# Optimization experiments

Measured on AMD Instinct MI355X. Metric: run time of the kernel, lower is better.

The kernel has to match this reference:

```python
import jax, jax.numpy as jnp
import numpy as np

# Object condensation loss config (matches init_kwargs / HGCalML defaults)
Q_MIN = 0.5
S_B = 1.0
POT_SCALE = 1.0
REP_SCALE = 1.0
BETA_SCALE = 1.0
E_WEIGHT = 1.0
HUBER_DELTA = 2.0
E_DEN_OFFSET = 1.0
K_MAX = 192          # object-id slots per event; id 0 = noise
EPS = 1e-6

B, N = 4, 50000


def setup_inputs() -> dict:
    key = jax.random.key(0)
    k1, k2, k3, k4, k5 = jax.random.split(key, 5)
    return {
        "beta": jax.random.uniform(k1, (B, N, 1), dtype=jnp.float32),
        "ccoords": jax.random.normal(k2, (B, N, 2), dtype=jnp.float32),
        "pred_energy": jax.random.uniform(k3, (B, N, 1), dtype=jnp.float32),
        "true_energy": jax.random.uniform(k4, (B, N, 1), dtype=jnp.float32),
        "truth_idx": jax.random.randint(k5, (B, N), 0, K_MAX, dtype=jnp.int32),
    }


def _per_event(beta, ccoords, pred_e, true_e, tidx):
    # beta: [N,1], ccoords: [N,2], tidx: [N] int (0 = noise)
    beta = jnp.clip(beta[:, 0], 1e-4, 1.0 - 1e-4)            # [N]
    q = jnp.arctanh(beta) ** 2 + Q_MIN                        # charge  [N]

    ids = jnp.arange(K_MAX)
    M = (tidx[:, None] == ids[None, :]) & (ids[None, :] > 0)  # [N,K] membership
    Mf = M.astype(q.dtype)
    obj_valid = jnp.any(M, axis=0)                            # [K]
    vf = obj_valid.astype(q.dtype)

    # condensation point alpha_k = argmax_q over members of object k
    qM = jnp.where(M, q[:, None], -1.0)                       # [N,K]
    idx_alpha = jnp.argmax(qM, axis=0)                        # [K]
    x_alpha = ccoords[idx_alpha]                              # [K,2]
    q_alpha = q[idx_alpha]                                    # [K]
    beta_alpha = beta[idx_alpha]                              # [K]

    # pairwise hit<->condensation-point distances
    d2 = jnp.sum((ccoords[:, None, :] - x_alpha[None, :, :]) ** 2, axis=-1)  # [N,K]

    # attractive potential (members), repulsive hinge (non-members of valid objects)
    att = jnp.sum(d2 * q_alpha[None, :] * Mf, axis=-1)                       # [N]
    dist = jnp.sqrt(d2 + EPS)
    rep = jnp.sum(jnp.maximum(0.0, 1.0 - dist) * q_alpha[None, :]
                  * (1.0 - Mf) * vf[None, :], axis=-1)                       # [N]
    L_V = jnp.mean(q * (POT_SCALE * att + REP_SCALE * rep))

    n_obj = jnp.sum(vf) + EPS
    L_beta = BETA_SCALE * jnp.sum((1.0 - beta_alpha) * vf) / n_obj

    noise = (tidx == 0).astype(q.dtype)
    L_noise = S_B * jnp.sum(beta * noise) / (jnp.sum(noise) + EPS)

    # energy payload loss: relative error, Huber, beta-weighted per object
    ediff = (pred_e[:, 0] - true_e[:, 0]) / (true_e[:, 0] + E_DEN_OFFSET)
    ad = jnp.abs(ediff)
    eh = jnp.where(ad <= HUBER_DELTA, 0.5 * ad ** 2,
                   HUBER_DELTA * (ad - 0.5 * HUBER_DELTA))                   # [N]
    pw = Mf * beta[:, None]                                                  # [N,K]
    per_obj_e = jnp.sum(pw * eh[:, None], axis=0) / (jnp.sum(pw, axis=0) + EPS)
    L_E = E_WEIGHT * jnp.sum(per_obj_e * vf) / n_obj

    return L_V + L_beta + L_noise + L_E


def reference(beta, ccoords, pred_energy, true_energy, truth_idx):
    per_ev = jax.vmap(_per_event)(beta, ccoords, pred_energy, true_energy, truth_idx)
    return jnp.mean(per_ev)
```

## Files before the change

kernel.cpp:

```cpp
#include <hip/hip_runtime.h>
#include <math.h>

#define KM 192
#define EPSF 1e-6f
#define QMIN 0.5f
#define BLKA 256
#define HA 4
#define TILEA (BLKA * HA)
#define BLKM 256
#define NTILES 128

__device__ __forceinline__ float clipb(float b) {
    return fminf(fmaxf(b, 1e-4f), 1.0f - 1e-4f);
}
__device__ __forceinline__ float fast_atanh(float b) {
    float r = (1.f + b) * __builtin_amdgcn_rcpf(1.f - b);
    return 0.34657359f * __builtin_amdgcn_logf(r);
}
__device__ __forceinline__ float bcast(float v, int j) {
    return __int_as_float(__builtin_amdgcn_readlane(__float_as_int(v), j));
}

__global__ void __launch_bounds__(BLKA)
k_amax(const float* __restrict__ beta, const int* __restrict__ tidx,
       unsigned long long* __restrict__ pscr, int N, int HBT) {
    const int e = blockIdx.y;
    __shared__ unsigned long long smax[KM];
    for (int k = threadIdx.x; k < KM; k += BLKA) smax[k] = 0ull;
    __syncthreads();
    const size_t base = (size_t)e * N;
    #pragma unroll
    for (int h = 0; h < HA; ++h) {
        int i = blockIdx.x * TILEA + h * BLKA + threadIdx.x;
        if (i < N) {
            int t = tidx[base + i];
            if (t > 0) {
                float bc = clipb(beta[base + i]);
                unsigned long long pack =
                    ((unsigned long long)__float_as_uint(bc) << 32) |
                    (unsigned long long)(unsigned)(N - 1 - i);
                atomicMax(&smax[t], pack);
            }
        }
    }
    __syncthreads();
    unsigned long long* row = pscr + ((size_t)e * HBT + blockIdx.x) * KM;
    for (int k = threadIdx.x; k < KM; k += BLKA) row[k] = smax[k];
}

__global__ void __launch_bounds__(256)
k_alpha(const unsigned long long* __restrict__ pscr, const float* __restrict__ cc,
        float4* __restrict__ alpha, float* __restrict__ abw,
        float* __restrict__ enm, float* __restrict__ eden,
        float* __restrict__ scal, int N, int HBT) {
    const int e = blockIdx.x;
    const int k = threadIdx.x;
    if (k < KM) {
        const unsigned long long* pk = pscr + (size_t)e * HBT * KM + k;
        unsigned long long v = 0ull;
        #pragma unroll 8
        for (int t = 0; t < HBT; ++t) {
            unsigned long long p = pk[(size_t)t * KM];
            if (p > v) v = p;
        }
        float4 a = make_float4(0.f, 0.f, 0.f, 0.f);
        float bw = 0.f;
        if (v) {
            int idx = N - 1 - (int)(unsigned)(v & 0xffffffffull);
            bw = __uint_as_float((unsigned)(v >> 32));
            float at = fast_atanh(bw);
            float2 cp = ((const float2*)cc)[(size_t)e * N + idx];
            a.x = cp.x; a.y = cp.y;
            a.z = fmaf(at, at, QMIN);
        }
        alpha[e * KM + k] = a;
        abw  [e * KM + k] = bw;
    }
    for (int z = threadIdx.x; z < KM; z += 256) {
        enm [e * KM + z] = 0.f;
        eden[e * KM + z] = 0.f;
    }
    if (threadIdx.x < 8) scal[e * 8 + threadIdx.x] = 0.f;
}

__global__ void __launch_bounds__(BLKM, 4)
k_main(const float* __restrict__ beta, const float* __restrict__ cc,
       const float* __restrict__ pe,   const float* __restrict__ te,
       const int* __restrict__ tidx,   const float4* __restrict__ alpha,
       float* __restrict__ enm, float* __restrict__ eden,
       float* __restrict__ scal, int N) {
    const int e = blockIdx.y;
    const int lane = threadIdx.x & 63;
    __shared__ float sn[KM], sd[KM];
    __shared__ float sw[12];
    for (int k = threadIdx.x; k < KM; k += BLKM) { sn[k] = 0.f; sd[k] = 0.f; }

    const float4* __restrict__ ae = alpha + e * KM;
    const float4 o0 = ae[lane];
    const float4 o1 = ae[lane + 64];
    const float4 o2 = ae[lane + 128];
    __syncthreads();

    const size_t base = (size_t)e * N;
    const int hpt   = (N + NTILES - 1) / NTILES;
    const int start = blockIdx.x * hpt;
    const int end   = min(start + hpt, N);
    const int nst   = (hpt + BLKM - 1) / BLKM;

    float r0 = 0.f, r1 = 0.f, r2 = 0.f;
    float lvh = 0.f, bn = 0.f, cn = 0.f;

    for (int s = 0; s < nst; ++s) {
        const int i = start + s * BLKM + (int)threadIdx.x;
        const bool ok = i < end;
        const size_t ii = base + (ok ? i : 0);
        const float2 cp = ((const float2*)cc)[ii];
        const float  bc = clipb(beta[ii]);
        const int    t  = ok ? tidx[ii] : -1;
        const float  at = fast_atanh(bc);
        const float  qh = ok ? fmaf(at, at, QMIN) : 0.f;

        if (t > 0) {
            float4 av = ae[t];
            float dx = cp.x - av.x, dy = cp.y - av.y;
            float d2 = fmaf(dx, dx, dy * dy);
            float hin = fmaxf(1.f - __builtin_amdgcn_sqrtf(d2 + EPSF), 0.f);
            lvh = fmaf(qh * av.z, d2 - hin, lvh);
            float tev = te[ii];
            float edv = (pe[ii] - tev) * __builtin_amdgcn_rcpf(tev + 1.f);
            float ad  = fabsf(edv);
            float eh  = (ad <= 2.f) ? 0.5f * ad * ad : 2.f * (ad - 1.f);
            atomicAdd(&sn[t], bc * eh);
            atomicAdd(&sd[t], bc);
        } else if (t == 0) { bn += bc; cn += 1.f; }

        #pragma unroll 16
        for (int j = 0; j < 64; ++j) {
            const float xh = bcast(cp.x, j);
            const float yh = bcast(cp.y, j);
            const float qb = bcast(qh,  j);
            float dx0 = o0.x - xh, dy0 = o0.y - yh;
            float dx1 = o1.x - xh, dy1 = o1.y - yh;
            float dx2 = o2.x - xh, dy2 = o2.y - yh;
            float d0 = fmaf(dx0, dx0, fmaf(dy0, dy0, EPSF));
            float d1 = fmaf(dx1, dx1, fmaf(dy1, dy1, EPSF));
            float d2 = fmaf(dx2, dx2, fmaf(dy2, dy2, EPSF));
            r0 = fmaf(fmaxf(1.f - __builtin_amdgcn_sqrtf(d0), 0.f), qb, r0);
            r1 = fmaf(fmaxf(1.f - __builtin_amdgcn_sqrtf(d1), 0.f), qb, r1);
            r2 = fmaf(fmaxf(1.f - __builtin_amdgcn_sqrtf(d2), 0.f), qb, r2);
        }
    }

    float lv = fmaf(o0.z, r0, fmaf(o1.z, r1, fmaf(o2.z, r2, lvh)));
    __syncthreads();

    if (threadIdx.x < KM) {
        float vd = sd[threadIdx.x];
        if (vd != 0.f) {
            atomicAdd(&enm [e * KM + threadIdx.x], sn[threadIdx.x]);
            atomicAdd(&eden[e * KM + threadIdx.x], vd);
        }
    }
    for (int off = 32; off > 0; off >>= 1) {
        lv += __shfl_down(lv, off);
        bn += __shfl_down(bn, off);
        cn += __shfl_down(cn, off);
    }
    const int wid = threadIdx.x >> 6;
    if ((threadIdx.x & 63) == 0) { sw[wid] = lv; sw[4 + wid] = bn; sw[8 + wid] = cn; }
    __syncthreads();
    if (threadIdx.x == 0) {
        atomicAdd(&scal[e * 8 + 0], (sw[0] + sw[1]) + (sw[2] + sw[3]));
        atomicAdd(&scal[e * 8 + 3], (sw[4] + sw[5]) + (sw[6] + sw[7]));
        atomicAdd(&scal[e * 8 + 4], (sw[8] + sw[9]) + (sw[10] + sw[11]));
    }
}

__global__ void __launch_bounds__(256)
k_fin(const float* __restrict__ enm, const float* __restrict__ eden,
      const float* __restrict__ abw, const float* __restrict__ scal,
      float* __restrict__ out, int N, int B) {
    __shared__ float sred[12];
    const int wid = threadIdx.x >> 6;
    float tot = 0.f;
    for (int ev = 0; ev < B; ++ev) {
        float lb = 0.f, nv = 0.f, le = 0.f;
        if (threadIdx.x < KM) {
            float bw = abw[ev * KM + threadIdx.x];
            if (bw > 0.f) {
                lb = 1.f - bw;
                nv = 1.f;
                le = enm[ev * KM + threadIdx.x] / (eden[ev * KM + threadIdx.x] + EPSF);
            }
        }
        for (int off = 32; off > 0; off >>= 1) {
            lb += __shfl_down(lb, off);
            nv += __shfl_down(nv, off);
            le += __shfl_down(le, off);
        }
        if ((threadIdx.x & 63) == 0) { sred[wid] = lb; sred[4 + wid] = nv; sred[8 + wid] = le; }
        __syncthreads();
        if (threadIdx.x == 0) {
            float lbs = (sred[0] + sred[1]) + (sred[2] + sred[3]);
            float nvs = (sred[4] + sred[5]) + (sred[6] + sred[7]);
            float les = (sred[8] + sred[9]) + (sred[10] + sred[11]);
            float nobj = nvs + EPSF;
            tot += scal[ev * 8 + 0] / (float)N + lbs / nobj
                 + scal[ev * 8 + 3] / (scal[ev * 8 + 4] + EPSF) + les / nobj;
        }
        __syncthreads();
    }
    if (threadIdx.x == 0) out[0] = tot / (float)B;
}

extern "C" void kernel_launch(void* const* d_in, const int* in_sizes, int n_in,
                              void* d_out, int out_size, void* d_ws, size_t ws_size,
                              hipStream_t stream) {
    const int B = 4;
    const int N = in_sizes[0] / B;
    const int HBT = (N + TILEA - 1) / TILEA;

    const float* beta = (const float*)d_in[0];
    const float* cc   = (const float*)d_in[1];
    const float* pe   = (const float*)d_in[2];
    const float* te   = (const float*)d_in[3];
    const int*   tidx = (const int*)  d_in[4];
    float* out = (float*)d_out;

    char* ws = (char*)d_ws;
    unsigned long long* pscr = (unsigned long long*)ws;
    float4* alpha = (float4*)(ws + (size_t)B * HBT * KM * 8);
    float*  abw   = (float*)(alpha + B * KM);
    float*  enm   = abw  + B * KM;
    float*  eden  = enm  + B * KM;
    float*  scal  = eden + B * KM;

    k_amax<<<dim3(HBT, B), dim3(BLKA), 0, stream>>>(beta, tidx, pscr, N, HBT);
    k_alpha<<<dim3(B), dim3(256), 0, stream>>>(pscr, cc, alpha, abw, enm, eden, scal, N, HBT);
    k_main<<<dim3(NTILES, B), dim3(BLKM), 0, stream>>>(
        beta, cc, pe, te, tidx, alpha, enm, eden, scal, N);
    k_fin<<<dim3(1), dim3(256), 0, stream>>>(enm, eden, abw, scal, out, N, B);
}
```

Measured before the change: 102.7 us.

## Restructure into pre-pass plus fused main kernel with last-block finalize

Moves energy and noise accumulation into the argmax pre-pass, which now reduces condensation-point packs with global atomicMax, and drops the separate alpha and finalize kernels. The main kernel rebuilds alpha in shared memory per block and uses one block per 256 hits instead of a fixed tile count with strided loops. A last-block counter handles the final reduction. The aim is to cut launches and improve parallelism. The cost is a memset, redundant alpha decoding in every block and more global atomics.

New measurement: 95.27 us. 7.2% less time.

```diff
diff --git a/kernel.cpp b/kernel.cpp
--- a/kernel.cpp
+++ b/kernel.cpp
@@ -4,11 +4,9 @@
 #define KM 192
 #define EPSF 1e-6f
 #define QMIN 0.5f
-#define BLKA 256
+#define BLK 256
 #define HA 4
-#define TILEA (BLKA * HA)
-#define BLKM 256
-#define NTILES 128
+#define TILEA (BLK * HA)
 
 __device__ __forceinline__ float clipb(float b) {
     return fminf(fmaxf(b, 1e-4f), 1.0f - 1e-4f);
@@ -21,140 +19,46 @@
     return __int_as_float(__builtin_amdgcn_readlane(__float_as_int(v), j));
 }
 
-__global__ void __launch_bounds__(BLKA)
-k_amax(const float* __restrict__ beta, const int* __restrict__ tidx,
-       unsigned long long* __restrict__ pscr, int N, int HBT) {
+__global__ void __launch_bounds__(BLK)
+k_pre(const float* __restrict__ beta, const int* __restrict__ tidx,
+      const float* __restrict__ pe,   const float* __restrict__ te,
+      unsigned long long* __restrict__ packs,
+      float* __restrict__ enm, float* __restrict__ eden,
+      float* __restrict__ scal, int N) {
     const int e = blockIdx.y;
     __shared__ unsigned long long smax[KM];
-    for (int k = threadIdx.x; k < KM; k += BLKA) smax[k] = 0ull;
-    __syncthreads();
+    __shared__ float sn[KM], sd[KM];
+    __shared__ float sw[8];
+    if (threadIdx.x < KM) { smax[threadIdx.x] = 0ull; sn[threadIdx.x] = 0.f; sd[threadIdx.x] = 0.f; }
+    __syncthreads();
+
     const size_t base = (size_t)e * N;
+    float bn = 0.f, cn = 0.f;
     #pragma unroll
     for (int h = 0; h < HA; ++h) {
-        int i = blockIdx.x * TILEA + h * BLKA + threadIdx.x;
+        int i = blockIdx.x * TILEA + h * BLK + threadIdx.x;
         if (i < N) {
-            int t = tidx[base + i];
+            int   t  = tidx[base + i];
+            float bc = clipb(beta[base + i]);
             if (t > 0) {
-                float bc = clipb(beta[base + i]);
                 unsigned long long pack =
                     ((unsigned long long)__float_as_uint(bc) << 32) |
                     (unsigned long long)(unsigned)(N - 1 - i);
                 atomicMax(&smax[t], pack);
-            }
-        }
-    }
-    __syncthreads();
-    unsigned long long* row = pscr + ((size_t)e * HBT + blockIdx.x) * KM;
-    for (int k = threadIdx.x; k < KM; k += BLKA) row[k] = smax[k];
-}
-
-__global__ void __launch_bounds__(256)
-k_alpha(const unsigned long long* __restrict__ pscr, const float* __restrict__ cc,
-        float4* __restrict__ alpha, float* __restrict__ abw,
-        float* __restrict__ enm, float* __restrict__ eden,
-        float* __restrict__ scal, int N, int HBT) {
-    const int e = blockIdx.x;
-    const int k = threadIdx.x;
-    if (k < KM) {
-        const unsigned long long* pk = pscr + (size_t)e * HBT * KM + k;
-        unsigned long long v = 0ull;
-        #pragma unroll 8
-        for (int t = 0; t < HBT; ++t) {
-            unsigned long long p = pk[(size_t)t * KM];
-            if (p > v) v = p;
-        }
-        float4 a = make_float4(0.f, 0.f, 0.f, 0.f);
-        float bw = 0.f;
-        if (v) {
-            int idx = N - 1 - (int)(unsigned)(v & 0xffffffffull);
-            bw = __uint_as_float((unsigned)(v >> 32));
-            float at = fast_atanh(bw);
-            float2 cp = ((const float2*)cc)[(size_t)e * N + idx];
-            a.x = cp.x; a.y = cp.y;
-            a.z = fmaf(at, at, QMIN);
-        }
-        alpha[e * KM + k] = a;
-        abw  [e * KM + k] = bw;
-    }
-    for (int z = threadIdx.x; z < KM; z += 256) {
-        enm [e * KM + z] = 0.f;
-        eden[e * KM + z] = 0.f;
-    }
-    if (threadIdx.x < 8) scal[e * 8 + threadIdx.x] = 0.f;
-}
-
-__global__ void __launch_bounds__(BLKM, 4)
-k_main(const float* __restrict__ beta, const float* __restrict__ cc,
-       const float* __restrict__ pe,   const float* __restrict__ te,
-       const int* __restrict__ tidx,   const float4* __restrict__ alpha,
-       float* __restrict__ enm, float* __restrict__ eden,
-       float* __restrict__ scal, int N) {
-    const int e = blockIdx.y;
-    const int lane = threadIdx.x & 63;
-    __shared__ float sn[KM], sd[KM];
-    __shared__ float sw[12];
-    for (int k = threadIdx.x; k < KM; k += BLKM) { sn[k] = 0.f; sd[k] = 0.f; }
-
-    const float4* __restrict__ ae = alpha + e * KM;
-    const float4 o0 = ae[lane];
-    const float4 o1 = ae[lane + 64];
-    const float4 o2 = ae[lane + 128];
-    __syncthreads();
-
-    const size_t base = (size_t)e * N;
-    const int hpt   = (N + NTILES - 1) / NTILES;
-    const int start = blockIdx.x * hpt;
-    const int end   = min(start + hpt, N);
-    const int nst   = (hpt + BLKM - 1) / BLKM;
-
-    float r0 = 0.f, r1 = 0.f, r2 = 0.f;
-    float lvh = 0.f, bn = 0.f, cn = 0.f;
-
-    for (int s = 0; s < nst; ++s) {
-        const int i = start + s * BLKM + (int)threadIdx.x;
-        const bool ok = i < end;
-        const size_t ii = base + (ok ? i : 0);
-        const float2 cp = ((const float2*)cc)[ii];
-        const float  bc = clipb(beta[ii]);
-        const int    t  = ok ? tidx[ii] : -1;
-        const float  at = fast_atanh(bc);
-        const float  qh = ok ? fmaf(at, at, QMIN) : 0.f;
-
-        if (t > 0) {
-            float4 av = ae[t];
-            float dx = cp.x - av.x, dy = cp.y - av.y;
-            float d2 = fmaf(dx, dx, dy * dy);
-            float hin = fmaxf(1.f - __builtin_amdgcn_sqrtf(d2 + EPSF), 0.f);
-            lvh = fmaf(qh * av.z, d2 - hin, lvh);
-            float tev = te[ii];
-            float edv = (pe[ii] - tev) * __builtin_amdgcn_rcpf(tev + 1.f);
-            float ad  = fabsf(edv);
-            float eh  = (ad <= 2.f) ? 0.5f * ad * ad : 2.f * (ad - 1.f);
-            atomicAdd(&sn[t], bc * eh);
-            atomicAdd(&sd[t], bc);
-        } else if (t == 0) { bn += bc; cn += 1.f; }
-
-        #pragma unroll 16
-        for (int j = 0; j < 64; ++j) {
-            const float xh = bcast(cp.x, j);
-            const float yh = bcast(cp.y, j);
-            const float qb = bcast(qh,  j);
-            float dx0 = o0.x - xh, dy0 = o0.y - yh;
-            float dx1 = o1.x - xh, dy1 = o1.y - yh;
-            float dx2 = o2.x - xh, dy2 = o2.y - yh;
-            float d0 = fmaf(dx0, dx0, fmaf(dy0, dy0, EPSF));
-            float d1 = fmaf(dx1, dx1, fmaf(dy1, dy1, EPSF));
-            float d2 = fmaf(dx2, dx2, fmaf(dy2, dy2, EPSF));
-            r0 = fmaf(fmaxf(1.f - __builtin_amdgcn_sqrtf(d0), 0.f), qb, r0);
-            r1 = fmaf(fmaxf(1.f - __builtin_amdgcn_sqrtf(d1), 0.f), qb, r1);
-            r2 = fmaf(fmaxf(1.f - __builtin_amdgcn_sqrtf(d2), 0.f), qb, r2);
-        }
-    }
-
-    float lv = fmaf(o0.z, r0, fmaf(o1.z, r1, fmaf(o2.z, r2, lvh)));
+                float tev = te[base + i];
+                float edv = (pe[base + i] - tev) * __builtin_amdgcn_rcpf(tev + 1.f);
+                float ad  = fabsf(edv);
+                float eh  = (ad <= 2.f) ? 0.5f * ad * ad : 2.f * (ad - 1.f);
+                atomicAdd(&sn[t], bc * eh);
+                atomicAdd(&sd[t], bc);
+            } else { bn += bc; cn += 1.f; }
+        }
+    }
     __syncthreads();
 
     if (threadIdx.x < KM) {
+        unsigned long long v = smax[threadIdx.x];
+        if (v) atomicMax(&packs[e * KM + threadIdx.x], v);
         float vd = sd[threadIdx.x];
         if (vd != 0.f) {
             atomicAdd(&enm [e * KM + threadIdx.x], sn[threadIdx.x]);
@@ -162,31 +66,112 @@
         }
     }
     for (int off = 32; off > 0; off >>= 1) {
-        lv += __shfl_down(lv, off);
         bn += __shfl_down(bn, off);
         cn += __shfl_down(cn, off);
     }
     const int wid = threadIdx.x >> 6;
-    if ((threadIdx.x & 63) == 0) { sw[wid] = lv; sw[4 + wid] = bn; sw[8 + wid] = cn; }
+    if ((threadIdx.x & 63) == 0) { sw[wid] = bn; sw[4 + wid] = cn; }
     __syncthreads();
     if (threadIdx.x == 0) {
+        atomicAdd(&scal[e * 8 + 3], (sw[0] + sw[1]) + (sw[2] + sw[3]));
+        atomicAdd(&scal[e * 8 + 4], (sw[4] + sw[5]) + (sw[6] + sw[7]));
+    }
+}
+
+__global__ void __launch_bounds__(BLK, 4)
+k_main(const float* __restrict__ beta, const float* __restrict__ cc,
+       const int* __restrict__ tidx,
+       const unsigned long long* __restrict__ packs,
+       float* __restrict__ abw,
+       const float* __restrict__ enm, const float* __restrict__ eden,
+       float* __restrict__ scal, unsigned int* __restrict__ cnt,
+       float* __restrict__ out, int N, int B) {
+    const int e = blockIdx.y;
+    __shared__ float4 sa[KM];
+    __shared__ float  sw[12];
+    __shared__ int    lastFlag;
+
+    if (threadIdx.x < KM) {
+        unsigned long long v = packs[e * KM + threadIdx.x];
+        float4 a = make_float4(0.f, 0.f, 0.f, 0.f);
+        if (v) {
+            int idx  = N - 1 - (int)(unsigned)(v & 0xffffffffull);
+            float bw = __uint_as_float((unsigned)(v >> 32));
+            float at = fast_atanh(bw);
+            float2 cp = ((const float2*)cc)[(size_t)e * N + idx];
+            a = make_float4(cp.x, cp.y, fmaf(at, at, QMIN), bw);
+        }
+        sa[threadIdx.x] = a;
+        if (blockIdx.x == 0) abw[e * KM + threadIdx.x] = a.w;
+    }
+    __syncthreads();
+
+    const int lane = threadIdx.x & 63;
+    const float4 o0 = sa[lane];
+    const float4 o1 = sa[lane + 64];
+    const float4 o2 = sa[lane + 128];
+
+    const size_t base = (size_t)e * N;
+    const int i = blockIdx.x * BLK + threadIdx.x;
+    const bool ok = i < N;
+    const size_t ii = base + (ok ? i : 0);
+    const float2 cp = ((const float2*)cc)[ii];
+    const float  bc = clipb(beta[ii]);
+    const int    t  = ok ? tidx[ii] : -1;
+    const float  at = fast_atanh(bc);
+    const float  qh = ok ? fmaf(at, at, QMIN) : 0.f;
+
+    float lvh = 0.f;
+    if (t > 0) {
+        float4 av = sa[t];
+        float dx = cp.x - av.x, dy = cp.y - av.y;
+        float d2 = fmaf(dx, dx, dy * dy);
+        float hin = fmaxf(1.f - __builtin_amdgcn_sqrtf(d2 + EPSF), 0.f);
+        lvh = qh * av.z * (d2 - hin);
+    }
+
+    float r0 = 0.f, r1 = 0.f, r2 = 0.f;
+    #pragma unroll 16
+    for (int j = 0; j < 64; ++j) {
+        const float xh = bcast(cp.x, j);
+        const float yh = bcast(cp.y, j);
+        const float qb = bcast(qh,  j);
+        float dx0 = o0.x - xh, dy0 = o0.y - yh;
+        float dx1 = o1.x - xh, dy1 = o1.y - yh;
+        float dx2 = o2.x - xh, dy2 = o2.y - yh;
+        float d0 = fmaf(dx0, dx0, fmaf(dy0, dy0, EPSF));
+        float d1 = fmaf(dx1, dx1, fmaf(dy1, dy1, EPSF));
+        float d2 = fmaf(dx2, dx2, fmaf(dy2, dy2, EPSF));
+        r0 = fmaf(fmaxf(1.f - __builtin_amdgcn_sqrtf(d0), 0.f), qb, r0);
+        r1 = fmaf(fmaxf(1.f - __builtin_amdgcn_sqrtf(d1), 0.f), qb, r1);
+        r2 = fmaf(fmaxf(1.f - __builtin_amdgcn_sqrtf(d2), 0.f), qb, r2);
+    }
+    float lv = fmaf(o0.z, r0, fmaf(o1.z, r1, fmaf(o2.z, r2, lvh)));
+    __syncthreads();
+
+    for (int off = 32; off > 0; off >>= 1) lv += __shfl_down(lv, off);
+    const int wid = threadIdx.x >> 6;
+    if ((threadIdx.x & 63) == 0) sw[wid] = lv;
+    __syncthreads();
+    if (threadIdx.x == 0)
         atomicAdd(&scal[e * 8 + 0], (sw[0] + sw[1]) + (sw[2] + sw[3]));
-        atomicAdd(&scal[e * 8 + 3], (sw[4] + sw[5]) + (sw[6] + sw[7]));
-        atomicAdd(&scal[e * 8 + 4], (sw[8] + sw[9]) + (sw[10] + sw[11]));
-    }
-}
-
-__global__ void __launch_bounds__(256)
-k_fin(const float* __restrict__ enm, const float* __restrict__ eden,
-      const float* __restrict__ abw, const float* __restrict__ scal,
-      float* __restrict__ out, int N, int B) {
-    __shared__ float sred[12];
-    const int wid = threadIdx.x >> 6;
+
+    if (threadIdx.x == 0) {
+        __threadfence();
+        unsigned int old = atomicAdd(&cnt[0], 1u);
+        lastFlag = (old == gridDim.x * gridDim.y - 1u);
+    }
+    __syncthreads();
+    if (!lastFlag) return;
+    __threadfence();
+
+    volatile float* vab = abw;
+    volatile float* vsc = scal;
     float tot = 0.f;
     for (int ev = 0; ev < B; ++ev) {
         float lb = 0.f, nv = 0.f, le = 0.f;
         if (threadIdx.x < KM) {
-            float bw = abw[ev * KM + threadIdx.x];
+            float bw = vab[ev * KM + threadIdx.x];
             if (bw > 0.f) {
                 lb = 1.f - bw;
                 nv = 1.f;
@@ -198,15 +183,15 @@
             nv += __shfl_down(nv, off);
             le += __shfl_down(le, off);
         }
-        if ((threadIdx.x & 63) == 0) { sred[wid] = lb; sred[4 + wid] = nv; sred[8 + wid] = le; }
+        if ((threadIdx.x & 63) == 0) { sw[wid] = lb; sw[4 + wid] = nv; sw[8 + wid] = le; }
         __syncthreads();
         if (threadIdx.x == 0) {
-            float lbs = (sred[0] + sred[1]) + (sred[2] + sred[3]);
-            float nvs = (sred[4] + sred[5]) + (sred[6] + sred[7]);
-            float les = (sred[8] + sred[9]) + (sred[10] + sred[11]);
+            float lbs = (sw[0] + sw[1]) + (sw[2] + sw[3]);
+            float nvs = (sw[4] + sw[5]) + (sw[6] + sw[7]);
+            float les = (sw[8] + sw[9]) + (sw[10] + sw[11]);
             float nobj = nvs + EPSF;
-            tot += scal[ev * 8 + 0] / (float)N + lbs / nobj
-                 + scal[ev * 8 + 3] / (scal[ev * 8 + 4] + EPSF) + les / nobj;
+            tot += vsc[ev * 8 + 0] / (float)N + lbs / nobj
+                 + vsc[ev * 8 + 3] / (vsc[ev * 8 + 4] + EPSF) + les / nobj;
         }
         __syncthreads();
     }
@@ -219,6 +204,7 @@
     const int B = 4;
     const int N = in_sizes[0] / B;
     const int HBT = (N + TILEA - 1) / TILEA;
+    const int MB  = (N + BLK - 1) / BLK;
 
     const float* beta = (const float*)d_in[0];
     const float* cc   = (const float*)d_in[1];
@@ -228,16 +214,16 @@
     float* out = (float*)d_out;
 
     char* ws = (char*)d_ws;
-    unsigned long long* pscr = (unsigned long long*)ws;
-    float4* alpha = (float4*)(ws + (size_t)B * HBT * KM * 8);
-    float*  abw   = (float*)(alpha + B * KM);
-    float*  enm   = abw  + B * KM;
-    float*  eden  = enm  + B * KM;
-    float*  scal  = eden + B * KM;
-
-    k_amax<<<dim3(HBT, B), dim3(BLKA), 0, stream>>>(beta, tidx, pscr, N, HBT);
-    k_alpha<<<dim3(B), dim3(256), 0, stream>>>(pscr, cc, alpha, abw, enm, eden, scal, N, HBT);
-    k_main<<<dim3(NTILES, B), dim3(BLKM), 0, stream>>>(
-        beta, cc, pe, te, tidx, alpha, enm, eden, scal, N);
-    k_fin<<<dim3(1), dim3(256), 0, stream>>>(enm, eden, abw, scal, out, N, B);
-}
+    unsigned long long* packs = (unsigned long long*)ws;
+    float* abw  = (float*)(ws + (size_t)B * KM * 8);
+    float* enm  = abw  + B * KM;
+    float* eden = enm  + B * KM;
+    float* scal = eden + B * KM;
+    unsigned int* cnt = (unsigned int*)(scal + B * 8);
+    const size_t zeroBytes = (char*)(cnt + 16) - ws;
+
+    (void)hipMemsetAsync(d_ws, 0, zeroBytes, stream);
+    k_pre<<<dim3(HBT, B), dim3(BLK), 0, stream>>>(beta, tidx, pe, te, packs, enm, eden, scal, N);
+    k_main<<<dim3(MB, B), dim3(BLK), 0, stream>>>(
+        beta, cc, tidx, packs, abw, enm, eden, scal, cnt, out, N, B);
+}
```
